# Optimization experiments

Hardware: AMD Instinct MI355X
Metric: run time of the kernel (lower is better)

Reference implementation:

```python
import jax, jax.numpy as jnp
import numpy as np

F, OUT = 256, 16
H = [128, 128, 64]
B = 8192


def _normed(v, g):
    # weight_norm (torch default dim=0): w[o,:] = g[o] * v[o,:] / ||v[o,:]||
    # v: [F, out, in], g: [F, out]
    return g[..., None] * v / jnp.linalg.norm(v, axis=-1, keepdims=True)


def setup_inputs() -> dict:
    key = jax.random.key(0)
    ks = jax.random.split(key, 12)
    s = 0.1
    return {
        "tabular": jax.random.normal(ks[0], (B, 2, F), dtype=jnp.float32),
        # input layer: Linear(1, H[0]) per feature, stacked over F
        "v_in": jax.random.normal(ks[1], (F, H[0], 1), dtype=jnp.float32) * s,
        "g_in": jnp.ones((F, H[0]), dtype=jnp.float32),
        "b_in": jax.random.normal(ks[2], (F, H[0]), dtype=jnp.float32) * s,
        # dense_0: Linear(H[0], H[1])
        "v_h0": jax.random.normal(ks[3], (F, H[1], H[0]), dtype=jnp.float32) * s,
        "g_h0": jnp.ones((F, H[1]), dtype=jnp.float32),
        "b_h0": jax.random.normal(ks[4], (F, H[1]), dtype=jnp.float32) * s,
        # dense_1: Linear(H[1], H[2])
        "v_h1": jax.random.normal(ks[5], (F, H[2], H[1]), dtype=jnp.float32) * s,
        "g_h1": jnp.ones((F, H[2]), dtype=jnp.float32),
        "b_h1": jax.random.normal(ks[6], (F, H[2]), dtype=jnp.float32) * s,
        # dense_out: Linear(H[2], OUT, bias=False)
        "v_out": jax.random.normal(ks[7], (F, OUT, H[2]), dtype=jnp.float32) * s,
        "g_out": jnp.ones((F, OUT), dtype=jnp.float32),
        "bias": jnp.zeros((1, OUT), dtype=jnp.float32),
    }


def reference(tabular, v_in, g_in, b_in, v_h0, g_h0, b_h0, v_h1, g_h1, b_h1,
              v_out, g_out, bias):
    values, is_missing = tabular[:, 0, :], tabular[:, 1, :]  # [B, F]
    x = values * (1.0 - is_missing)
    # input layer: in-dim is 1, so it's an outer product with the weight column
    w0 = _normed(v_in, g_in)[:, :, 0]                       # [F, H0]
    h = jax.nn.relu(x[:, :, None] * w0[None] + b_in[None])  # [B, F, H0]
    # hidden layers (dropout is identity in eval mode)
    h = jax.nn.relu(jnp.einsum("bfi,foi->bfo", h, _normed(v_h0, g_h0)) + b_h0[None])
    h = jax.nn.relu(jnp.einsum("bfi,foi->bfo", h, _normed(v_h1, g_h1)) + b_h1[None])
    outputs = jnp.einsum("bfi,foi->bfo", h, _normed(v_out, g_out))  # [B, F, OUT]
    # feature_dropout is identity in eval mode
    logits = jnp.sum(outputs, axis=1) + bias                # [B, OUT]
    return logits, outputs
```

## Files before the change

### kernel.cpp

```cpp
#include <hip/hip_runtime.h>

typedef unsigned short u16;
typedef unsigned int   u32;
typedef __attribute__((ext_vector_type(8))) short bf16x8;
typedef __attribute__((ext_vector_type(4))) float f32x4;
typedef __attribute__((ext_vector_type(2))) float f32x2;

#define NFEAT  256
#define NBATCH 8192
#define BT     128
#define NBT    (NBATCH / BT)
#define ITERS  8

__device__ __forceinline__ u16 f2bf(float f) {
    u32 u = __builtin_bit_cast(u32, f);
    return (u16)((u + 0x7FFFu + ((u >> 16) & 1u)) >> 16);
}
__device__ __forceinline__ u32 cvtpk(float a, float b) {
    u32 r;
    asm("v_cvt_pk_bf16_f32 %0, %1, %2" : "=v"(r) : "v"(a), "v"(b));
    return r;
}
__device__ __forceinline__ f32x4 mfma16(bf16x8 a, bf16x8 b, f32x4 c) {
    return __builtin_amdgcn_mfma_f32_16x16x32_bf16(a, b, c, 0, 0, 0);
}
__device__ __forceinline__ bf16x8 frag_word0(u32 word0) {
    union { bf16x8 v; u32 w[4]; } u;
    u.w[0] = word0; u.w[1] = 0; u.w[2] = 0; u.w[3] = 0;
    return u.v;
}
__device__ __forceinline__ char* swz(char* base, int b, int col2) {
    return base + b * 256 + (col2 ^ ((b & 15) << 4));
}
__device__ __forceinline__ const char* swz(const char* base, int b, int col2) {
    return base + b * 256 + (col2 ^ ((b & 15) << 4));
}
__device__ __forceinline__ uint2 relu_pk4(f32x4 v, f32x4 bs) {
    f32x4 s = v + bs;
    return make_uint2(cvtpk(fmaxf(s[0], 0.f), fmaxf(s[1], 0.f)),
                      cvtpk(fmaxf(s[2], 0.f), fmaxf(s[3], 0.f)));
}

__global__ void prep_w0(const float* __restrict__ v_in, const float* __restrict__ g_in,
                        u16* __restrict__ w0) {
    int i = blockIdx.x * blockDim.x + threadIdx.x;
    float v = v_in[i];
    float g = g_in[i];
    w0[i] = f2bf(v >= 0.f ? g : -g);
}

__global__ void prep_norm(const float* __restrict__ v_h0, const float* __restrict__ g_h0,
                          const float* __restrict__ v_h1, const float* __restrict__ g_h1,
                          const float* __restrict__ v_out, const float* __restrict__ g_out,
                          u16* __restrict__ w1, u16* __restrict__ w2, u16* __restrict__ w3) {
    const int wave = (blockIdx.x * blockDim.x + threadIdx.x) >> 6;
    const int lane = threadIdx.x & 63;
    if (wave < 32768 + 16384) {
        const float* src; u16* dst; float g;
        if (wave < 32768) {
            src = v_h0 + (size_t)wave * 128; dst = w1 + (size_t)wave * 128; g = g_h0[wave];
        } else {
            int r = wave - 32768;
            src = v_h1 + (size_t)r * 128; dst = w2 + (size_t)r * 128; g = g_h1[r];
        }
        f32x2 v = *(const f32x2*)(src + lane * 2);
        float ss = v[0] * v[0] + v[1] * v[1];
        #pragma unroll
        for (int off = 32; off; off >>= 1) ss += __shfl_xor(ss, off);
        float s = g * rsqrtf(ss);
        *(u32*)(dst + lane * 2) = cvtpk(v[0] * s, v[1] * s);
    } else {
        int r = wave - 49152;
        const float* src = v_out + (size_t)r * 64;
        float v = src[lane];
        float ss = v * v;
        #pragma unroll
        for (int off = 32; off; off >>= 1) ss += __shfl_xor(ss, off);
        float s = g_out[r] * rsqrtf(ss);
        w3[(size_t)r * 64 + lane] = f2bf(v * s);
    }
}

__global__ void prep_x(const float* __restrict__ tab, u16* __restrict__ x_t) {
    __shared__ u16 tile[64][65];
    const int bb = (blockIdx.x % (NBATCH / 64)) * 64;
    const int ff = (blockIdx.x / (NBATCH / 64)) * 64;
    const int tr = threadIdx.x >> 6;
    const int tc = threadIdx.x & 63;
    #pragma unroll
    for (int i = 0; i < 16; i++) {
        int b = bb + tr + i * 4;
        float val  = tab[(size_t)b * 512 + ff + tc];
        float miss = tab[(size_t)b * 512 + 256 + ff + tc];
        tile[tr + i * 4][tc] = f2bf(val * (1.f - miss));
    }
    __syncthreads();
    #pragma unroll
    for (int i = 0; i < 16; i++) {
        int fr = tr + i * 4;
        x_t[(size_t)(ff + fr) * NBATCH + bb + tc] = tile[tc][fr];
    }
}

__global__ void reduce_logits(const float* __restrict__ outputs,
                              const float* __restrict__ bias,
                              float* __restrict__ logits) {
    const int b = blockIdx.x * 4 + (threadIdx.x >> 6);
    const int lane = threadIdx.x & 63;
    const int j4 = lane & 3;
    const int fo = lane >> 2;
    const float* base = outputs + (size_t)b * (NFEAT * 16);
    f32x4 acc = {};
    #pragma unroll
    for (int it = 0; it < 16; it++) {
        f32x4 v = *(const f32x4*)(base + (fo + it * 16) * 16 + j4 * 4);
        acc[0] += v[0]; acc[1] += v[1]; acc[2] += v[2]; acc[3] += v[3];
    }
    #pragma unroll
    for (int off = 4; off < 64; off <<= 1) {
        acc[0] += __shfl_xor(acc[0], off);
        acc[1] += __shfl_xor(acc[1], off);
        acc[2] += __shfl_xor(acc[2], off);
        acc[3] += __shfl_xor(acc[3], off);
    }
    if (lane < 4) {
        f32x4 bs = *(const f32x4*)(bias + lane * 4);
        acc[0] += bs[0]; acc[1] += bs[1]; acc[2] += bs[2]; acc[3] += bs[3];
        *(f32x4*)(logits + b * 16 + lane * 4) = acc;
    }
}

__global__ __launch_bounds__(256, 2) void nam_main(
    const u16* __restrict__ x_t, const u16* __restrict__ w0g,
    const u16* __restrict__ w1g, const u16* __restrict__ w2g, const u16* __restrict__ w3g,
    const float* __restrict__ b_in, const float* __restrict__ b_h0, const float* __restrict__ b_h1,
    float* __restrict__ outputs)
{
    __shared__ u16 hA[BT * 128];
    __shared__ u16 hB[BT * 128];

    const int bid   = blockIdx.x;
    const int f     = (bid & 7) * 32 + ((bid >> 3) & 31);
    const int chunk = bid >> 8;
    const int t  = threadIdx.x;
    const int w  = t >> 6;
    const int wo = w >> 1;
    const int wb = w & 1;
    const int lane = t & 63;
    const int lo = lane & 15;
    const int hi = lane >> 4;

    bf16x8 a0f[4];
    #pragma unroll
    for (int m = 0; m < 4; m++) {
        const int o = f * 128 + wo * 64 + m * 16 + lo;
        float bi = b_in[o];
        u32 pk = (u32)w0g[o] | (cvtpk(bi, bi) << 16);
        a0f[m] = frag_word0(hi == 0 ? pk : 0u);
    }
    bf16x8 w1f[4][4];
    {
        const u16* base = w1g + ((size_t)(f * 128 + wo * 64 + lo)) * 128 + hi * 8;
        #pragma unroll
        for (int m = 0; m < 4; m++)
            #pragma unroll
            for (int ks = 0; ks < 4; ks++)
                w1f[m][ks] = *(const bf16x8*)(base + m * 2048 + ks * 32);
    }
    bf16x8 w2f[2][4];
    {
        const u16* base = w2g + ((size_t)(f * 64 + wo * 32 + lo)) * 128 + hi * 8;
        #pragma unroll
        for (int m = 0; m < 2; m++)
            #pragma unroll
            for (int ks = 0; ks < 4; ks++)
                w2f[m][ks] = *(const bf16x8*)(base + m * 2048 + ks * 32);
    }
    bf16x8 w3f[2];
    {
        const u16* base = w3g + ((size_t)(f * 16 + lo)) * 64 + hi * 8;
        #pragma unroll
        for (int ks = 0; ks < 2; ks++)
            w3f[ks] = *(const bf16x8*)(base + ks * 32);
    }
    f32x4 bs1[4];
    #pragma unroll
    for (int m = 0; m < 4; m++)
        bs1[m] = *(const f32x4*)(b_h0 + f * 128 + wo * 64 + m * 16 + hi * 4);
    f32x4 bs2[2];
    #pragma unroll
    for (int m = 0; m < 2; m++)
        bs2[m] = *(const f32x4*)(b_h1 + f * 64 + wo * 32 + m * 16 + hi * 4);

    const u16* xbase = x_t + (size_t)f * NBATCH;

    u32 xw[4];
    {
        const int bt0 = chunk * ITERS;
        #pragma unroll
        for (int n = 0; n < 4; n++)
            xw[n] = (u32)xbase[bt0 * BT + wb * 64 + n * 16 + lo];
    }

    for (int it = 0; it < ITERS; it++) {
        const int bt = chunk * ITERS + it;

        __syncthreads();

        {
            bf16x8 bm[4];
            #pragma unroll
            for (int n = 0; n < 4; n++)
                bm[n] = frag_word0(hi == 0 ? (xw[n] | 0x3F800000u) : 0u);
            #pragma unroll
            for (int m = 0; m < 4; m++) {
                #pragma unroll
                for (int n = 0; n < 4; n++) {
                    f32x4 d = mfma16(a0f[m], bm[n], f32x4{});
                    const int b = wb * 64 + n * 16 + lo;
                    const int col2 = (wo * 64 + m * 16 + hi * 4) * 2;
                    *(uint2*)swz((char*)hA, b, col2) =
                        make_uint2(cvtpk(fmaxf(0.f, d[0]), fmaxf(0.f, d[1])),
                                   cvtpk(fmaxf(0.f, d[2]), fmaxf(0.f, d[3])));
                }
            }
        }
        __syncthreads();

        {
            if (it + 1 < ITERS) {
                #pragma unroll
                for (int n = 0; n < 4; n++)
                    xw[n] = (u32)xbase[(bt + 1) * BT + wb * 64 + n * 16 + lo];
            }
            f32x4 acc[4][4] = {};
            #pragma unroll
            for (int ks = 0; ks < 4; ks++) {
                bf16x8 bm[4];
                #pragma unroll
                for (int n = 0; n < 4; n++) {
                    const int b = wb * 64 + n * 16 + lo;
                    bm[n] = *(const bf16x8*)swz((const char*)hA, b, ks * 64 + hi * 16);
                }
                __builtin_amdgcn_s_setprio(1);
                #pragma unroll
                for (int m = 0; m < 4; m++)
                    #pragma unroll
                    for (int n = 0; n < 4; n++)
                        acc[m][n] = mfma16(w1f[m][ks], bm[n], acc[m][n]);
                __builtin_amdgcn_s_setprio(0);
            }
            #pragma unroll
            for (int m = 0; m < 4; m++) {
                const int col2 = (wo * 64 + m * 16 + hi * 4) * 2;
                #pragma unroll
                for (int n = 0; n < 4; n++) {
                    const int b = wb * 64 + n * 16 + lo;
                    *(uint2*)swz((char*)hB, b, col2) = relu_pk4(acc[m][n], bs1[m]);
                }
            }
        }
        __syncthreads();

        {
            f32x4 acc[2][4] = {};
            #pragma unroll
            for (int ks = 0; ks < 4; ks++) {
                bf16x8 bm[4];
                #pragma unroll
                for (int n = 0; n < 4; n++) {
                    const int b = wb * 64 + n * 16 + lo;
                    bm[n] = *(const bf16x8*)swz((const char*)hB, b, ks * 64 + hi * 16);
                }
                __builtin_amdgcn_s_setprio(1);
                #pragma unroll
                for (int m = 0; m < 2; m++)
                    #pragma unroll
                    for (int n = 0; n < 4; n++)
                        acc[m][n] = mfma16(w2f[m][ks], bm[n], acc[m][n]);
                __builtin_amdgcn_s_setprio(0);
            }
            #pragma unroll
            for (int m = 0; m < 2; m++) {
                const int col2 = (wo * 32 + m * 16 + hi * 4) * 2;
                #pragma unroll
                for (int n = 0; n < 4; n++) {
                    const int b = wb * 64 + n * 16 + lo;
                    *(uint2*)swz((char*)hA, b, col2) = relu_pk4(acc[m][n], bs2[m]);
                }
            }
        }
        __syncthreads();

        {
            f32x4 acc[2] = {};
            #pragma unroll
            for (int ks = 0; ks < 2; ks++) {
                #pragma unroll
                for (int n = 0; n < 2; n++) {
                    const int b = w * 32 + n * 16 + lo;
                    bf16x8 bm = *(const bf16x8*)swz((const char*)hA, b, ks * 64 + hi * 16);
                    acc[n] = mfma16(w3f[ks], bm, acc[n]);
                }
            }
            #pragma unroll
            for (int n = 0; n < 2; n++) {
                const int gb = bt * BT + w * 32 + n * 16 + lo;
                float* op = outputs + ((size_t)gb * NFEAT + f) * 16 + hi * 4;
                *(f32x4*)op = acc[n];
            }
        }
    }
}

extern "C" void kernel_launch(void* const* d_in, const int* in_sizes, int n_in,
                              void* d_out, int out_size, void* d_ws, size_t ws_size,
                              hipStream_t stream) {
    const float* tab   = (const float*)d_in[0];
    const float* v_in  = (const float*)d_in[1];
    const float* g_in  = (const float*)d_in[2];
    const float* b_in  = (const float*)d_in[3];
    const float* v_h0  = (const float*)d_in[4];
    const float* g_h0  = (const float*)d_in[5];
    const float* b_h0  = (const float*)d_in[6];
    const float* v_h1  = (const float*)d_in[7];
    const float* g_h1  = (const float*)d_in[8];
    const float* b_h1  = (const float*)d_in[9];
    const float* v_out = (const float*)d_in[10];
    const float* g_out = (const float*)d_in[11];
    const float* bias  = (const float*)d_in[12];

    char* ws = (char*)d_ws;
    u16* w0  = (u16*)(ws);
    u16* w1  = (u16*)(ws + 65536);
    u16* w2  = (u16*)(ws + 65536 + 8388608);
    u16* w3  = (u16*)(ws + 12648448);
    u16* x_t = (u16*)(ws + 13172736);

    float* logits  = (float*)d_out;
    float* outputs = (float*)d_out + (size_t)NBATCH * 16;

    hipLaunchKernelGGL(prep_w0,   dim3(128),   dim3(256), 0, stream, v_in, g_in, w0);
    hipLaunchKernelGGL(prep_norm, dim3(13312), dim3(256), 0, stream,
                       v_h0, g_h0, v_h1, g_h1, v_out, g_out, w1, w2, w3);
    hipLaunchKernelGGL(prep_x,    dim3(512),   dim3(256), 0, stream, tab, x_t);
    hipLaunchKernelGGL(nam_main,  dim3(NFEAT * NBT / ITERS), dim3(256), 0, stream,
                       x_t, w0, w1, w2, w3, b_in, b_h0, b_h1, outputs);
    hipLaunchKernelGGL(reduce_logits, dim3(NBATCH / 4), dim3(256), 0, stream,
                       outputs, bias, logits);
}
```

Baseline: 182.3 us.

## Switch hidden-layer matmuls from 16x16x32 to 32x32x16 MFMA tiles

Replaces the 16x16x32 bf16 MFMA instructions with 32x32x16 MFMA in the input, first and second hidden layers. Weight fragments and LDS activation reads and writes are re-indexed for the 32-row layout, and bias vectors are now loaded inside the epilogue instead of being held in registers. Larger tiles mean fewer MFMA issues and fewer LDS fragment loads per FLOP. In exchange the epilogue uses more scattered stores and bias reloads, and register pressure may shift under launch_bounds(256,2).

New measurement: 203.2 us. 1.11x slower.

```diff
diff --git a/kernel.cpp b/kernel.cpp
--- a/kernel.cpp
+++ b/kernel.cpp
@@ -2,9 +2,10 @@
 
 typedef unsigned short u16;
 typedef unsigned int   u32;
-typedef __attribute__((ext_vector_type(8))) short bf16x8;
-typedef __attribute__((ext_vector_type(4))) float f32x4;
-typedef __attribute__((ext_vector_type(2))) float f32x2;
+typedef __attribute__((ext_vector_type(8)))  short bf16x8;
+typedef __attribute__((ext_vector_type(4)))  float f32x4;
+typedef __attribute__((ext_vector_type(2)))  float f32x2;
+typedef __attribute__((ext_vector_type(16))) float f32x16;
 
 #define NFEAT  256
 #define NBATCH 8192
@@ -24,6 +25,9 @@
 __device__ __forceinline__ f32x4 mfma16(bf16x8 a, bf16x8 b, f32x4 c) {
     return __builtin_amdgcn_mfma_f32_16x16x32_bf16(a, b, c, 0, 0, 0);
 }
+__device__ __forceinline__ f32x16 mfma32(bf16x8 a, bf16x8 b, f32x16 c) {
+    return __builtin_amdgcn_mfma_f32_32x32x16_bf16(a, b, c, 0, 0, 0);
+}
 __device__ __forceinline__ bf16x8 frag_word0(u32 word0) {
     union { bf16x8 v; u32 w[4]; } u;
     u.w[0] = word0; u.w[1] = 0; u.w[2] = 0; u.w[3] = 0;
@@ -34,11 +38,6 @@
 }
 __device__ __forceinline__ const char* swz(const char* base, int b, int col2) {
     return base + b * 256 + (col2 ^ ((b & 15) << 4));
-}
-__device__ __forceinline__ uint2 relu_pk4(f32x4 v, f32x4 bs) {
-    f32x4 s = v + bs;
-    return make_uint2(cvtpk(fmaxf(s[0], 0.f), fmaxf(s[1], 0.f)),
-                      cvtpk(fmaxf(s[2], 0.f), fmaxf(s[3], 0.f)));
 }
 
 __global__ void prep_w0(const float* __restrict__ v_in, const float* __restrict__ g_in,
@@ -147,34 +146,34 @@
     const int wo = w >> 1;
     const int wb = w & 1;
     const int lane = t & 63;
-    const int lo = lane & 15;
-    const int hi = lane >> 4;
-
-    bf16x8 a0f[4];
-    #pragma unroll
-    for (int m = 0; m < 4; m++) {
-        const int o = f * 128 + wo * 64 + m * 16 + lo;
+    const int lo  = lane & 15;
+    const int hi  = lane >> 4;
+    const int l31 = lane & 31;
+    const int l5  = lane >> 5;
+
+    bf16x8 a0f[2];
+    #pragma unroll
+    for (int mo = 0; mo < 2; mo++) {
+        const int o = f * 128 + wo * 64 + mo * 32 + l31;
         float bi = b_in[o];
         u32 pk = (u32)w0g[o] | (cvtpk(bi, bi) << 16);
-        a0f[m] = frag_word0(hi == 0 ? pk : 0u);
-    }
-    bf16x8 w1f[4][4];
+        a0f[mo] = frag_word0(l5 == 0 ? pk : 0u);
+    }
+    bf16x8 w1f[2][8];
     {
-        const u16* base = w1g + ((size_t)(f * 128 + wo * 64 + lo)) * 128 + hi * 8;
-        #pragma unroll
-        for (int m = 0; m < 4; m++)
-            #pragma unroll
-            for (int ks = 0; ks < 4; ks++)
-                w1f[m][ks] = *(const bf16x8*)(base + m * 2048 + ks * 32);
-    }
-    bf16x8 w2f[2][4];
+        const u16* base = w1g + ((size_t)(f * 128 + wo * 64 + l31)) * 128 + l5 * 8;
+        #pragma unroll
+        for (int mo = 0; mo < 2; mo++)
+            #pragma unroll
+            for (int ks = 0; ks < 8; ks++)
+                w1f[mo][ks] = *(const bf16x8*)(base + mo * 4096 + ks * 16);
+    }
+    bf16x8 w2f[8];
     {
-        const u16* base = w2g + ((size_t)(f * 64 + wo * 32 + lo)) * 128 + hi * 8;
-        #pragma unroll
-        for (int m = 0; m < 2; m++)
-            #pragma unroll
-            for (int ks = 0; ks < 4; ks++)
-                w2f[m][ks] = *(const bf16x8*)(base + m * 2048 + ks * 32);
+        const u16* base = w2g + ((size_t)(f * 64 + wo * 32 + l31)) * 128 + l5 * 8;
+        #pragma unroll
+        for (int ks = 0; ks < 8; ks++)
+            w2f[ks] = *(const bf16x8*)(base + ks * 16);
     }
     bf16x8 w3f[2];
     {
@@ -183,23 +182,15 @@
         for (int ks = 0; ks < 2; ks++)
             w3f[ks] = *(const bf16x8*)(base + ks * 32);
     }
-    f32x4 bs1[4];
-    #pragma unroll
-    for (int m = 0; m < 4; m++)
-        bs1[m] = *(const f32x4*)(b_h0 + f * 128 + wo * 64 + m * 16 + hi * 4);
-    f32x4 bs2[2];
-    #pragma unroll
-    for (int m = 0; m < 2; m++)
-        bs2[m] = *(const f32x4*)(b_h1 + f * 64 + wo * 32 + m * 16 + hi * 4);
 
     const u16* xbase = x_t + (size_t)f * NBATCH;
 
-    u32 xw[4];
+    u32 xw[2];
     {
         const int bt0 = chunk * ITERS;
         #pragma unroll
-        for (int n = 0; n < 4; n++)
-            xw[n] = (u32)xbase[bt0 * BT + wb * 64 + n * 16 + lo];
+        for (int n = 0; n < 2; n++)
+            xw[n] = (u32)xbase[bt0 * BT + wb * 64 + n * 32 + l31];
     }
 
     for (int it = 0; it < ITERS; it++) {
@@ -208,20 +199,23 @@
         __syncthreads();
 
         {
-            bf16x8 bm[4];
-            #pragma unroll
-            for (int n = 0; n < 4; n++)
-                bm[n] = frag_word0(hi == 0 ? (xw[n] | 0x3F800000u) : 0u);
-            #pragma unroll
-            for (int m = 0; m < 4; m++) {
-                #pragma unroll
-                for (int n = 0; n < 4; n++) {
-                    f32x4 d = mfma16(a0f[m], bm[n], f32x4{});
-                    const int b = wb * 64 + n * 16 + lo;
-                    const int col2 = (wo * 64 + m * 16 + hi * 4) * 2;
-                    *(uint2*)swz((char*)hA, b, col2) =
-                        make_uint2(cvtpk(fmaxf(0.f, d[0]), fmaxf(0.f, d[1])),
-                                   cvtpk(fmaxf(0.f, d[2]), fmaxf(0.f, d[3])));
+            bf16x8 bm[2];
+            #pragma unroll
+            for (int n = 0; n < 2; n++)
+                bm[n] = frag_word0(l5 == 0 ? (xw[n] | 0x3F800000u) : 0u);
+            #pragma unroll
+            for (int mo = 0; mo < 2; mo++) {
+                #pragma unroll
+                for (int n = 0; n < 2; n++) {
+                    f32x16 d = mfma32(a0f[mo], bm[n], f32x16{});
+                    const int b = wb * 64 + n * 32 + l31;
+                    #pragma unroll
+                    for (int q = 0; q < 4; q++) {
+                        const int col2 = (wo * 64 + mo * 32 + q * 8 + l5 * 4) * 2;
+                        u32 p0 = cvtpk(fmaxf(0.f, d[q * 4 + 0]), fmaxf(0.f, d[q * 4 + 1]));
+                        u32 p1 = cvtpk(fmaxf(0.f, d[q * 4 + 2]), fmaxf(0.f, d[q * 4 + 3]));
+                        *(uint2*)swz((char*)hA, b, col2) = make_uint2(p0, p1);
+                    }
                 }
             }
         }
@@ -230,63 +224,78 @@
         {
             if (it + 1 < ITERS) {
                 #pragma unroll
-                for (int n = 0; n < 4; n++)
-                    xw[n] = (u32)xbase[(bt + 1) * BT + wb * 64 + n * 16 + lo];
-            }
-            f32x4 acc[4][4] = {};
-            #pragma unroll
-            for (int ks = 0; ks < 4; ks++) {
-                bf16x8 bm[4];
-                #pragma unroll
-                for (int n = 0; n < 4; n++) {
-                    const int b = wb * 64 + n * 16 + lo;
-                    bm[n] = *(const bf16x8*)swz((const char*)hA, b, ks * 64 + hi * 16);
+                for (int n = 0; n < 2; n++)
+                    xw[n] = (u32)xbase[(bt + 1) * BT + wb * 64 + n * 32 + l31];
+            }
+            f32x16 acc[2][2] = {};
+            #pragma unroll
+            for (int ks = 0; ks < 8; ks++) {
+                bf16x8 bm[2];
+                #pragma unroll
+                for (int n = 0; n < 2; n++) {
+                    const int b = wb * 64 + n * 32 + l31;
+                    bm[n] = *(const bf16x8*)swz((const char*)hA, b, ks * 32 + l5 * 16);
                 }
                 __builtin_amdgcn_s_setprio(1);
                 #pragma unroll
-                for (int m = 0; m < 4; m++)
+                for (int mo = 0; mo < 2; mo++)
                     #pragma unroll
-                    for (int n = 0; n < 4; n++)
-                        acc[m][n] = mfma16(w1f[m][ks], bm[n], acc[m][n]);
+                    for (int n = 0; n < 2; n++)
+                        acc[mo][n] = mfma32(w1f[mo][ks], bm[n], acc[mo][n]);
                 __builtin_amdgcn_s_setprio(0);
             }
             #pragma unroll
-            for (int m = 0; m < 4; m++) {
-                const int col2 = (wo * 64 + m * 16 + hi * 4) * 2;
-                #pragma unroll
-                for (int n = 0; n < 4; n++) {
-                    const int b = wb * 64 + n * 16 + lo;
-                    *(uint2*)swz((char*)hB, b, col2) = relu_pk4(acc[m][n], bs1[m]);
+            for (int mo = 0; mo < 2; mo++) {
+                #pragma unroll
+                for (int q = 0; q < 4; q++) {
+                    const int o = wo * 64 + mo * 32 + q * 8 + l5 * 4;
+                    f32x4 bs = *(const f32x4*)(b_h0 + f * 128 + o);
+                    #pragma unroll
+                    for (int n = 0; n < 2; n++) {
+                        const int b = wb * 64 + n * 32 + l31;
+                        float s0 = acc[mo][n][q * 4 + 0] + bs[0];
+                        float s1 = acc[mo][n][q * 4 + 1] + bs[1];
+                        float s2 = acc[mo][n][q * 4 + 2] + bs[2];
+                        float s3 = acc[mo][n][q * 4 + 3] + bs[3];
+                        u32 p0 = cvtpk(fmaxf(s0, 0.f), fmaxf(s1, 0.f));
+                        u32 p1 = cvtpk(fmaxf(s2, 0.f), fmaxf(s3, 0.f));
+                        *(uint2*)swz((char*)hB, b, o * 2) = make_uint2(p0, p1);
+                    }
                 }
             }
         }
         __syncthreads();
 
         {
-            f32x4 acc[2][4] = {};
-            #pragma unroll
-            for (int ks = 0; ks < 4; ks++) {
-                bf16x8 bm[4];
-                #pragma unroll
-                for (int n = 0; n < 4; n++) {
-                    const int b = wb * 64 + n * 16 + lo;
-                    bm[n] = *(const bf16x8*)swz((const char*)hB, b, ks * 64 + hi * 16);
+            f32x16 acc[2] = {};
+            #pragma unroll
+            for (int ks = 0; ks < 8; ks++) {
+                bf16x8 bm[2];
+                #pragma unroll
+                for (int n = 0; n < 2; n++) {
+                    const int b = wb * 64 + n * 32 + l31;
+                    bm[n] = *(const bf16x8*)swz((const char*)hB, b, ks * 32 + l5 * 16);
                 }
                 __builtin_amdgcn_s_setprio(1);
                 #pragma unroll
-                for (int m = 0; m < 2; m++)
-                    #pragma unroll
-                    for (int n = 0; n < 4; n++)
-                        acc[m][n] = mfma16(w2f[m][ks], bm[n], acc[m][n]);
+                for (int n = 0; n < 2; n++)
+                    acc[n] = mfma32(w2f[ks], bm[n], acc[n]);
                 __builtin_amdgcn_s_setprio(0);
             }
             #pragma unroll
-            for (int m = 0; m < 2; m++) {
-                const int col2 = (wo * 32 + m * 16 + hi * 4) * 2;
-                #pragma unroll
-                for (int n = 0; n < 4; n++) {
-                    const int b = wb * 64 + n * 16 + lo;
-                    *(uint2*)swz((char*)hA, b, col2) = relu_pk4(acc[m][n], bs2[m]);
+            for (int q = 0; q < 4; q++) {
+                const int o = wo * 32 + q * 8 + l5 * 4;
+                f32x4 bs = *(const f32x4*)(b_h1 + f * 64 + o);
+                #pragma unroll
+                for (int n = 0; n < 2; n++) {
+                    const int b = wb * 64 + n * 32 + l31;
+                    float s0 = acc[n][q * 4 + 0] + bs[0];
+                    float s1 = acc[n][q * 4 + 1] + bs[1];
+                    float s2 = acc[n][q * 4 + 2] + bs[2];
+                    float s3 = acc[n][q * 4 + 3] + bs[3];
+                    u32 p0 = cvtpk(fmaxf(s0, 0.f), fmaxf(s1, 0.f));
+                    u32 p1 = cvtpk(fmaxf(s2, 0.f), fmaxf(s3, 0.f));
+                    *(uint2*)swz((char*)hA, b, o * 2) = make_uint2(p0, p1);
                 }
             }
         }
```
